# Kernel tuning notes

Measured on AMD Instinct MI355X. Metric: run time of the kernel, lower is better.

Reference implementation:

```python
import jax, jax.numpy as jnp
import numpy as np

N, E, F_IN, HID, OUT, H = 50000, 500000, 128, 64, 64, 2
P_DROP = 0.2


def setup_inputs() -> dict:
    key = jax.random.key(0)
    ks = jax.random.split(key, 24)
    g = lambda k, shp: jax.random.normal(k, shp, jnp.float32) * 0.05
    inp = {
        "feat": jax.random.normal(ks[0], (N, F_IN), jnp.float32),
        "edge_src": jax.random.randint(ks[1], (E,), 0, N, jnp.int32),
        "edge_dst": jax.random.randint(ks[2], (E,), 0, N, jnp.int32),
        # feature-mask linears
        "Wmt": g(ks[3], (F_IN, F_IN)), "bmt": g(ks[4], (F_IN,)),
        "Wms": g(ks[5], (F_IN, F_IN)), "bms": g(ks[6], (F_IN,)),
        # SAGEConv layers (mean aggregator): self + neigh linear + bias
        "W1_self": g(ks[7], (F_IN, HID)), "W1_neigh": g(ks[8], (F_IN, HID)), "b1": g(ks[9], (HID,)),
        "W2_self": g(ks[10], (HID, OUT)), "W2_neigh": g(ks[11], (HID, OUT)), "b2": g(ks[12], (OUT,)),
        # GATv2Conv layers: fc_src, fc_dst, attn vector per head, bias
        "g1_Wsrc": g(ks[13], (F_IN, H * HID)), "g1_Wdst": g(ks[14], (F_IN, H * HID)),
        "g1_attn": g(ks[15], (H, HID)), "g1_bias": g(ks[16], (H * HID,)),
        "g2_Wsrc": g(ks[17], (HID, H * OUT)), "g2_Wdst": g(ks[18], (HID, H * OUT)),
        "g2_attn": g(ks[19], (H, OUT)), "g2_bias": g(ks[20], (H * OUT,)),
        # final projection
        "W3": g(ks[21], (OUT + F_IN, OUT)), "b3": g(ks[22], (OUT,)),
    }
    # deterministic (inverted) dropout masks, training=True, p=0.2
    keep = 1.0 - P_DROP
    km1, km2 = jax.random.split(ks[23])
    inp["drop_t"] = jax.random.bernoulli(km1, keep, (N, HID)).astype(jnp.float32) / keep
    inp["drop_s"] = jax.random.bernoulli(km2, keep, (N, HID)).astype(jnp.float32) / keep
    return inp


def _sage_mean(h, src, dst, W_self, W_neigh, b):
    # mean over in-neighbors, then linear (mean and linear commute)
    agg = jax.ops.segment_sum(h[src], dst, num_segments=N)          # [N,D]
    deg = jax.ops.segment_sum(jnp.ones((E,), h.dtype), dst, num_segments=N)
    h_neigh = agg / jnp.maximum(deg, 1.0)[:, None]
    return h @ W_self + h_neigh @ W_neigh + b


def _gatv2(h, src, dst, Wsrc, Wdst, attn, bias, heads, dout):
    fs = (h @ Wsrc).reshape(N, heads, dout)
    fd = (h @ Wdst).reshape(N, heads, dout)
    e = jax.nn.leaky_relu(fs[src] + fd[dst], 0.2)                   # [E,H,D]
    logits = jnp.einsum('ehd,hd->eh', e, attn)                      # [E,H]
    m = jax.ops.segment_max(logits, dst, num_segments=N)            # edge softmax per dst
    ex = jnp.exp(logits - m[dst])
    denom = jax.ops.segment_sum(ex, dst, num_segments=N)
    alpha = ex / denom[dst]                                         # [E,H]
    out = jax.ops.segment_sum(alpha[:, :, None] * fs[src], dst, num_segments=N)
    return out + bias.reshape(heads, dout)                          # [N,H,D]


def _l2norm(x):
    return x / jnp.maximum(jnp.linalg.norm(x, axis=1, keepdims=True), 1e-12)


def reference(feat, edge_src, edge_dst, Wmt, bmt, Wms, bms,
              W1_self, W1_neigh, b1, W2_self, W2_neigh, b2,
              g1_Wsrc, g1_Wdst, g1_attn, g1_bias,
              g2_Wsrc, g2_Wdst, g2_attn, g2_bias,
              W3, b3, drop_t, drop_s):
    gelu = lambda x: jax.nn.gelu(x, approximate=False)  # torch F.gelu default = exact erf
    # topology branch (SAGE)
    h_t = feat * jax.nn.sigmoid(feat @ Wmt + bmt)
    h_t = gelu(_sage_mean(h_t, edge_src, edge_dst, W1_self, W1_neigh, b1)) * drop_t
    h_t = gelu(_sage_mean(h_t, edge_src, edge_dst, W2_self, W2_neigh, b2))
    h_t = jnp.concatenate([h_t, feat], axis=1) @ W3 + b3
    h_t = _l2norm(jax.nn.leaky_relu(h_t, 0.01))
    # semantic branch (GATv2)
    h_s = feat * jax.nn.sigmoid(feat @ Wms + bms)
    h_s = gelu(_gatv2(h_s, edge_src, edge_dst, g1_Wsrc, g1_Wdst, g1_attn, g1_bias, H, HID)).mean(axis=1) * drop_s
    h_s = gelu(_gatv2(h_s, edge_src, edge_dst, g2_Wsrc, g2_Wdst, g2_attn, g2_bias, H, OUT)).mean(axis=1)
    h_s = _l2norm(h_s)
    return (h_t, h_s)
```

## Files before the change

### kernel.cpp

```cpp
#include <hip/hip_runtime.h>
#include <math.h>

constexpr int N_  = 50000;
constexpr int E_  = 500000;
constexpr int NB_ = (N_ + 255) / 256;

typedef unsigned short u16;
typedef unsigned int u32;
typedef short short8 __attribute__((ext_vector_type(8)));
typedef __bf16 bf16x8 __attribute__((ext_vector_type(8)));
typedef float f32x4 __attribute__((ext_vector_type(4)));
typedef short short4v __attribute__((ext_vector_type(4)));

#define DINL __device__ __forceinline__

DINL float gelu_f(float x) { return 0.5f * x * (1.f + erff(x * 0.70710678118654752f)); }
DINL float sigmoid_f(float x) { return 1.f / (1.f + expf(-x)); }
DINL u16 f2b(float x) {
  unsigned u = __float_as_uint(x);
  return (u16)((u + 0x7FFFu + ((u >> 16) & 1u)) >> 16);
}
DINL float b2f(u16 b) { return __uint_as_float(((unsigned)b) << 16); }

template <int CTRL>
DINL float dpp_add(float c) {
  int p = __builtin_amdgcn_update_dpp(0, __builtin_bit_cast(int, c), CTRL, 0xf, 0xf, false);
  return c + __builtin_bit_cast(float, p);
}
DINL float reduce16(float c) {
  c = dpp_add<0xB1>(c);
  c = dpp_add<0x4E>(c);
  c = dpp_add<0x141>(c);
  c = dpp_add<0x140>(c);
  return c;
}

__global__ void deg_int_kernel(const int* __restrict__ dst, int* __restrict__ deg) {
  int t = blockIdx.x * 256 + threadIdx.x;
  if (t < E_) atomicAdd(&deg[dst[t]], 1);
}

__global__ __launch_bounds__(256) void scan_local(const int* __restrict__ deg,
    int* __restrict__ rowptr, int* __restrict__ bsum) {
  __shared__ int sums[4];
  const int tid = threadIdx.x, lane = tid & 63, wid = tid >> 6;
  const int i = blockIdx.x * 256 + tid;
  int v = (i < N_) ? deg[i] : 0;
  int x = v;
#pragma unroll
  for (int o = 1; o < 64; o <<= 1) { int y = __shfl_up(x, o); if (lane >= o) x += y; }
  if (lane == 63) sums[wid] = x;
  __syncthreads();
  int woff = 0;
#pragma unroll
  for (int w = 0; w < 3; ++w) if (w < wid) woff += sums[w];
  if (i < N_) rowptr[i] = x - v + woff;
  if (tid == 255) bsum[blockIdx.x] = woff + x;
}

__global__ __launch_bounds__(256) void scan_block(const int* __restrict__ bsum,
                                                  int* __restrict__ bpre) {
  __shared__ int sums[4];
  const int tid = threadIdx.x, lane = tid & 63, wid = tid >> 6;
  int v = (tid < NB_) ? bsum[tid] : 0;
  int x = v;
#pragma unroll
  for (int o = 1; o < 64; o <<= 1) { int y = __shfl_up(x, o); if (lane >= o) x += y; }
  if (lane == 63) sums[wid] = x;
  __syncthreads();
  int woff = 0;
#pragma unroll
  for (int w = 0; w < 3; ++w) if (w < wid) woff += sums[w];
  if (tid < NB_) bpre[tid] = x - v + woff;
  if (tid == 255) bpre[NB_] = woff + x;
}

__global__ __launch_bounds__(256) void scan_add(int* __restrict__ rowptr,
                                                const int* __restrict__ bpre) {
  int i = blockIdx.x * 256 + threadIdx.x;
  if (i < N_) rowptr[i] += bpre[i >> 8];
  else if (i == N_) rowptr[N_] = bpre[NB_];
}

__global__ void csr_fill(const int* __restrict__ src, const int* __restrict__ dst,
                         const int* __restrict__ rowptr, int* __restrict__ cursor,
                         int* __restrict__ colsrc) {
  int e = blockIdx.x * 256 + threadIdx.x;
  if (e >= E_) return;
  int d = dst[e];
  int pos = rowptr[d] + atomicAdd(&cursor[d], 1);
  colsrc[pos] = src[e];
}

__global__ __launch_bounds__(256) void pack_feat(const float* __restrict__ f,
                                                 u16* __restrict__ o) {
  int t = blockIdx.x * 256 + threadIdx.x;
  float4 v = ((const float4*)f)[t];
  short4v r;
  r[0] = (short)f2b(v.x); r[1] = (short)f2b(v.y);
  r[2] = (short)f2b(v.z); r[3] = (short)f2b(v.w);
  ((short4v*)o)[t] = r;
}

__global__ __launch_bounds__(256) void pack_w(
    const float* __restrict__ Wmt, const float* __restrict__ Wms,
    const float* __restrict__ W1s, const float* __restrict__ W1n,
    const float* __restrict__ W2s, const float* __restrict__ W2n,
    const float* __restrict__ g1Ws, const float* __restrict__ g1Wd,
    const float* __restrict__ g2Ws, const float* __restrict__ g2Wd,
    const float* __restrict__ W3, u16* __restrict__ dst) {
  int e = blockIdx.x * 256 + threadIdx.x;
  const float *Wa, *Wb = nullptr;
  int K1, K2 = 0, Ca, Cb = 0, st;
  if (e < 16384)       { Wa = Wmt;  K1 = 128; Ca = 128;           st = 0; }
  else if (e < 32768)  { Wa = Wms;  K1 = 128; Ca = 128;           st = 16384; }
  else if (e < 49152)  { Wa = W1s;  Wb = W1n; K1 = 128; Ca = 64; Cb = 64; st = 32768; }
  else if (e < 57344)  { Wa = W2s;  Wb = W2n; K1 = 64;  Ca = 64; Cb = 64; st = 49152; }
  else if (e < 90112)  { Wa = g1Ws; Wb = g1Wd; K1 = 128; Ca = 128; Cb = 128; st = 57344; }
  else if (e < 106496) { Wa = g2Ws; Wb = g2Wd; K1 = 64;  Ca = 128; Cb = 128; st = 90112; }
  else                 { Wa = W3;   K1 = 192; Ca = 64;            st = 106496; }
  int el = e - st;
  int Kt = K1 + K2;
  int ct = el / (Kt * 16);
  int rem = el - ct * Kt * 16;
  int ks = rem >> 9, rem2 = rem & 511, lane = rem2 >> 3, j = rem2 & 7;
  int k = ks * 32 + ((lane >> 4) << 3) + j;
  int c = ct * 16 + (lane & 15);
  float v;
  if (k < K1) v = (c < Ca) ? Wa[k * Ca + c] : Wb[k * Cb + (c - Ca)];
  else        v = Wb[(k - K1) * Ca + c];
  dst[e] = f2b(v);
}

template <int K1, int K2, int C, int EPI>
__global__ __launch_bounds__(512) void gemm_mfma(
    const u16* __restrict__ A1, const u16* __restrict__ A2,
    const u16* __restrict__ Wp, const float* __restrict__ bias,
    const float* __restrict__ bias2, const float* __restrict__ mulf,
    void* __restrict__ outv, void* __restrict__ outv2) {
  constexpr int K = K1 + K2, KS = K / 32, CT4 = C / 64;
  constexpr int NCH1 = K1 / 8, NCH2 = K2 / 8;
  __shared__ u16 alds[64 * K];
  const int tid = threadIdx.x;
  const int w = tid >> 6, l = tid & 63;
  const int cq = w >> 1, rh = w & 1;
  const int wr0 = blockIdx.x * 64;

  short8 wfrag[KS][CT4];
#pragma unroll
  for (int ks = 0; ks < KS; ++ks)
#pragma unroll
    for (int c4 = 0; c4 < CT4; ++c4)
      wfrag[ks][c4] = *(const short8*)(Wp +
          ((size_t)((cq * CT4 + c4) * KS + ks) * 64 + l) * 8);

  for (int i = tid; i < 64 * NCH1; i += 512) {
    int rr = i / NCH1, kc = i % NCH1;
    int gr = wr0 + rr; if (gr >= N_) gr = N_ - 1;
    short8 v = *(const short8*)(A1 + (long)gr * K1 + kc * 8);
    *(short8*)&alds[rr * K + ((kc ^ (rr & 7)) << 3)] = v;
  }
  if constexpr (K2 > 0) {
    for (int i = tid; i < 64 * NCH2; i += 512) {
      int rr = i / NCH2, kc = i % NCH2;
      int gr = wr0 + rr; if (gr >= N_) gr = N_ - 1;
      short8 v = *(const short8*)(A2 + (long)gr * K2 + kc * 8);
      *(short8*)&alds[rr * K + (((NCH1 + kc) ^ (rr & 7)) << 3)] = v;
    }
  }
  __syncthreads();

  f32x4 acc[2][CT4];
#pragma unroll
  for (int rr = 0; rr < 2; ++rr)
#pragma unroll
    for (int c4 = 0; c4 < CT4; ++c4) acc[rr][c4] = (f32x4){0.f, 0.f, 0.f, 0.f};

#pragma unroll
  for (int ks = 0; ks < KS; ++ks) {
#pragma unroll
    for (int rr = 0; rr < 2; ++rr) {
      const int nr = (rh * 2 + rr) * 16 + (l & 15);
      const int ch = (ks * 4 + (l >> 4)) ^ (nr & 7);
      short8 av = *(const short8*)&alds[nr * K + (ch << 3)];
      bf16x8 bf = __builtin_bit_cast(bf16x8, av);
#pragma unroll
      for (int c4 = 0; c4 < CT4; ++c4)
        acc[rr][c4] = __builtin_amdgcn_mfma_f32_16x16x32_bf16(
            __builtin_bit_cast(bf16x8, wfrag[ks][c4]), bf, acc[rr][c4], 0, 0, 0);
    }
  }

  const int colq = (l >> 4) << 2;
  if constexpr (EPI == 0) {
    u16* out = (u16*)outv;
#pragma unroll
    for (int rr = 0; rr < 2; ++rr) {
      int row = wr0 + (rh * 2 + rr) * 16 + (l & 15);
      if (row >= N_) continue;
#pragma unroll
      for (int c4 = 0; c4 < CT4; ++c4) {
        int colb = (cq * CT4 + c4) * 16 + colq;
        short4v s;
#pragma unroll
        for (int r = 0; r < 4; ++r) s[r] = (short)f2b(acc[rr][c4][r]);
        *(short4v*)(out + (long)row * C + colb) = s;
      }
    }
  } else if constexpr (EPI == 4) {
    __shared__ float ssb[64][4];
    float* out = (float*)outv;
    const int colb = cq * 16 + colq;
    float4 bv = *(const float4*)(bias + colb);
    float xv[2][4];
#pragma unroll
    for (int rr = 0; rr < 2; ++rr) {
      float ss = 0.f;
#pragma unroll
      for (int r = 0; r < 4; ++r) {
        float x = acc[rr][0][r] + ((const float*)&bv)[r];
        x = fmaxf(x, 0.01f * x);
        xv[rr][r] = x; ss += x * x;
      }
      ss += __shfl_xor(ss, 16);
      ss += __shfl_xor(ss, 32);
      if (l < 16) ssb[(rh * 2 + rr) * 16 + l][cq] = ss;
    }
    __syncthreads();
#pragma unroll
    for (int rr = 0; rr < 2; ++rr) {
      int nl = (rh * 2 + rr) * 16 + (l & 15);
      int row = wr0 + nl;
      if (row >= N_) continue;
      float ss = ssb[nl][0] + ssb[nl][1] + ssb[nl][2] + ssb[nl][3];
      float sc = 1.f / fmaxf(sqrtf(ss), 1e-12f);
      float4 o;
#pragma unroll
      for (int r = 0; r < 4; ++r) ((float*)&o)[r] = xv[rr][r] * sc;
      *(float4*)(out + (long)row * 64 + colb) = o;
    }
  } else {
#pragma unroll
    for (int c4 = 0; c4 < CT4; ++c4) {
      const int ct = cq * CT4 + c4;
      const bool lo = ct < 8;
      u16* op = lo ? (u16*)outv : (u16*)outv2;
      const int ccb = (ct & 7) * 16 + colq;
      float4 bv = *(const float4*)((lo ? bias : bias2) + ccb);
#pragma unroll
      for (int rr = 0; rr < 2; ++rr) {
        int nl = (rh * 2 + rr) * 16 + (l & 15);
        int row = wr0 + nl;
        if (row >= N_) continue;
        int ch = (ccb >> 3) ^ (nl & 7);
        short4v fq = *(const short4v*)&alds[nl * K + (ch << 3) + (ccb & 7)];
        short4v s;
#pragma unroll
        for (int r = 0; r < 4; ++r) {
          float x = acc[rr][c4][r] + ((const float*)&bv)[r];
          float fv = b2f((u16)fq[r]);
          s[r] = (short)f2b(fv * sigmoid_f(x));
        }
        *(short4v*)(op + (long)row * 128 + ccb) = s;
      }
    }
  }
}

template <bool DROP>
__global__ __launch_bounds__(256) void gather_sage(const u16* __restrict__ qp,
    const int* __restrict__ rowptr, const int* __restrict__ colsrc,
    const float* __restrict__ bias, const float* __restrict__ drop,
    u16* __restrict__ out) {
  int node = blockIdx.x * 4 + (threadIdx.x >> 6);
  int l = threadIdx.x & 63;
  int ql = l & 15, qg = l >> 4;
  int beg = rowptr[node], end = rowptr[node + 1];
  const int off = 4 * ql;
  float a0 = 0.f, a1 = 0.f, a2 = 0.f, a3 = 0.f;
  float b0 = 0.f, b1 = 0.f, b2 = 0.f, b3 = 0.f;
  int j = beg;
  for (; j + 8 <= end; j += 8) {
    int s0 = colsrc[j + qg], s1 = colsrc[j + 4 + qg];
    uint2 v0 = *(const uint2*)(qp + (size_t)s0 * 128 + 64 + off);
    uint2 v1 = *(const uint2*)(qp + (size_t)s1 * 128 + 64 + off);
    a0 += b2f((u16)(v0.x & 0xffffu));
    a1 += b2f((u16)(v0.x >> 16));
    a2 += b2f((u16)(v0.y & 0xffffu));
    a3 += b2f((u16)(v0.y >> 16));
    b0 += b2f((u16)(v1.x & 0xffffu));
    b1 += b2f((u16)(v1.x >> 16));
    b2 += b2f((u16)(v1.y & 0xffffu));
    b3 += b2f((u16)(v1.y >> 16));
  }
  for (; j < end; j += 4) {
    int idx = j + qg;
    bool valid = idx < end;
    int s = colsrc[valid ? idx : end - 1];
    uint2 v = *(const uint2*)(qp + (size_t)s * 128 + 64 + off);
    if (!valid) { v.x = 0; v.y = 0; }
    a0 += b2f((u16)(v.x & 0xffffu));
    a1 += b2f((u16)(v.x >> 16));
    a2 += b2f((u16)(v.y & 0xffffu));
    a3 += b2f((u16)(v.y >> 16));
  }
  a0 += b0; a1 += b1; a2 += b2; a3 += b3;
  a0 += __shfl_xor(a0, 32); a1 += __shfl_xor(a1, 32);
  a2 += __shfl_xor(a2, 32); a3 += __shfl_xor(a3, 32);
  a0 += __shfl_xor(a0, 16); a1 += __shfl_xor(a1, 16);
  a2 += __shfl_xor(a2, 16); a3 += __shfl_xor(a3, 16);
  if (l < 16) {
    float inv = 1.f / fmaxf((float)(end - beg), 1.f);
    uint2 qv = *(const uint2*)(qp + (size_t)node * 128 + off);
    float4 bv = *(const float4*)(bias + off);
    float g0 = gelu_f(b2f((u16)(qv.x & 0xffffu)) + a0 * inv + bv.x);
    float g1 = gelu_f(b2f((u16)(qv.x >> 16))     + a1 * inv + bv.y);
    float g2 = gelu_f(b2f((u16)(qv.y & 0xffffu)) + a2 * inv + bv.z);
    float g3 = gelu_f(b2f((u16)(qv.y >> 16))     + a3 * inv + bv.w);
    if constexpr (DROP) {
      float4 dv = *(const float4*)(drop + (long)node * 64 + off);
      g0 *= dv.x; g1 *= dv.y; g2 *= dv.z; g3 *= dv.w;
    }
    short4v s;
    s[0] = (short)f2b(g0); s[1] = (short)f2b(g1);
    s[2] = (short)f2b(g2); s[3] = (short)f2b(g3);
    *(short4v*)(out + (long)node * 64 + off) = s;
  }
}

template <bool LAYER1>
__global__ __launch_bounds__(256) void gat_fused(const u16* __restrict__ fsfd,
    const int* __restrict__ rowptr, const int* __restrict__ colsrc,
    const float* __restrict__ attn, const float* __restrict__ bias,
    const float* __restrict__ drop, void* __restrict__ outv) {
  int node = blockIdx.x * 4 + (threadIdx.x >> 6);
  int l = threadIdx.x & 63;
  int hl = l & 31, half = l >> 5;
  const int off = 4 * hl;
  float4 av = *(const float4*)(attn + off);
  uint2 fdv = *(const uint2*)(fsfd + (size_t)node * 256 + 128 + off);
  float fd0 = b2f((u16)(fdv.x & 0xffffu)), fd1 = b2f((u16)(fdv.x >> 16));
  float fd2 = b2f((u16)(fdv.y & 0xffffu)), fd3 = b2f((u16)(fdv.y >> 16));
  float d_own = 0.f, acc0 = 0.f, acc1 = 0.f, acc2 = 0.f, acc3 = 0.f;

  auto edge = [&](uint2 v, float m) {
    float f0 = b2f((u16)(v.x & 0xffffu)), f1 = b2f((u16)(v.x >> 16));
    float f2 = b2f((u16)(v.y & 0xffffu)), f3 = b2f((u16)(v.y >> 16));
    float t0 = f0 + fd0, t1 = f1 + fd1, t2 = f2 + fd2, t3 = f3 + fd3;
    t0 = fmaxf(t0, 0.2f * t0); t1 = fmaxf(t1, 0.2f * t1);
    t2 = fmaxf(t2, 0.2f * t2); t3 = fmaxf(t3, 0.2f * t3);
    float c = t0 * av.x + t1 * av.y + t2 * av.z + t3 * av.w;
    c = reduce16(c);
    float e = __expf(c) * m;
    d_own += e;
    acc0 += e * f0; acc1 += e * f1; acc2 += e * f2; acc3 += e * f3;
  };

  const int beg = rowptr[node], end = rowptr[node + 1];
  int j = beg;
  for (; j + 8 <= end; j += 8) {
    int sa = colsrc[j + half],     sb = colsrc[j + 2 + half];
    int sc = colsrc[j + 4 + half], sd = colsrc[j + 6 + half];
    uint2 va = *(const uint2*)(fsfd + (size_t)sa * 256 + off);
    uint2 vb = *(const uint2*)(fsfd + (size_t)sb * 256 + off);
    uint2 vc = *(const uint2*)(fsfd + (size_t)sc * 256 + off);
    uint2 vd = *(const uint2*)(fsfd + (size_t)sd * 256 + off);
    edge(va, 1.f); edge(vb, 1.f); edge(vc, 1.f); edge(vd, 1.f);
  }
  for (; j < end; j += 2) {
    int idx = j + half;
    bool valid = idx < end;
    int s = colsrc[valid ? idx : end - 1];
    uint2 v = *(const uint2*)(fsfd + (size_t)s * 256 + off);
    if (!valid) { v.x = 0; v.y = 0; }
    edge(v, valid ? 1.f : 0.f);
  }

  acc0 += __shfl_xor(acc0, 32); acc1 += __shfl_xor(acc1, 32);
  acc2 += __shfl_xor(acc2, 32); acc3 += __shfl_xor(acc3, 32);
  d_own += __shfl_xor(d_own, 32);

  float4 bv = *(const float4*)(bias + off);
  float inv = d_own > 0.f ? 1.f / d_own : 0.f;
  float g0 = gelu_f(bv.x + acc0 * inv);
  float g1 = gelu_f(bv.y + acc1 * inv);
  float g2 = gelu_f(bv.z + acc2 * inv);
  float g3 = gelu_f(bv.w + acc3 * inv);
  float v0 = 0.5f * (g0 + __shfl_xor(g0, 16));
  float v1 = 0.5f * (g1 + __shfl_xor(g1, 16));
  float v2 = 0.5f * (g2 + __shfl_xor(g2, 16));
  float v3 = 0.5f * (g3 + __shfl_xor(g3, 16));
  if constexpr (LAYER1) {
    if (l < 16) {
      float4 dv = *(const float4*)(drop + (long)node * 64 + 4 * l);
      short4v s;
      s[0] = (short)f2b(v0 * dv.x); s[1] = (short)f2b(v1 * dv.y);
      s[2] = (short)f2b(v2 * dv.z); s[3] = (short)f2b(v3 * dv.w);
      *(short4v*)((u16*)outv + (long)node * 64 + 4 * l) = s;
    }
  } else {
    float ss = v0 * v0 + v1 * v1 + v2 * v2 + v3 * v3;
    ss = reduce16(ss);
    float sc = 1.f / fmaxf(sqrtf(ss), 1e-12f);
    if (l < 16) {
      float4 o; o.x = v0 * sc; o.y = v1 * sc; o.z = v2 * sc; o.w = v3 * sc;
      *(float4*)((float*)outv + (long)node * 64 + 4 * l) = o;
    }
  }
}

extern "C" void kernel_launch(void* const* d_in, const int* in_sizes, int n_in,
                              void* d_out, int out_size, void* d_ws, size_t ws_size,
                              hipStream_t stream) {
  const float* feat = (const float*)d_in[0];
  const int*   esrc = (const int*)d_in[1];
  const int*   edst = (const int*)d_in[2];
  const float* Wmt = (const float*)d_in[3],  *bmt = (const float*)d_in[4];
  const float* Wms = (const float*)d_in[5],  *bms = (const float*)d_in[6];
  const float* W1s = (const float*)d_in[7],  *W1n = (const float*)d_in[8],  *b1 = (const float*)d_in[9];
  const float* W2s = (const float*)d_in[10], *W2n = (const float*)d_in[11], *b2 = (const float*)d_in[12];
  const float* g1Ws = (const float*)d_in[13], *g1Wd = (const float*)d_in[14];
  const float* g1a  = (const float*)d_in[15], *g1b  = (const float*)d_in[16];
  const float* g2Ws = (const float*)d_in[17], *g2Wd = (const float*)d_in[18];
  const float* g2a  = (const float*)d_in[19], *g2b  = (const float*)d_in[20];
  const float* W3  = (const float*)d_in[21], *b3 = (const float*)d_in[22];
  const float* dropt = (const float*)d_in[23], *drops = (const float*)d_in[24];

  float* out_t = (float*)d_out;
  float* out_s = out_t + (long)N_ * 64;

  u16* wsh = (u16*)d_ws;
  u16* featbf = wsh;
  u16* hbuf_t = wsh +  6400000;
  u16* hbuf_s = wsh + 12800000;
  u16* qp1    = wsh + 19200000;
  u16* h1     = wsh + 25600000;
  u16* qp2    = wsh + 28800000;
  u16* h2     = wsh + 35200000;
  u16* hs1    = wsh + 38400000;
  u16* fsfd   = wsh + 41600000;
  u16* Wpk    = wsh + 54400000;
  int* degi   = (int*)(wsh + 54518784);
  int* cursor = degi + N_;
  int* rowptr = cursor + N_;
  int* colsrc = rowptr + N_ + 1;
  int* bsum   = colsrc + E_;
  int* bpre   = bsum + NB_;

  const u16* WpMT = Wpk;
  const u16* WpS1 = Wpk + 32768;
  const u16* WpS2 = Wpk + 49152;
  const u16* WpG1 = Wpk + 57344;
  const u16* WpG2 = Wpk + 90112;
  const u16* WpW3 = Wpk + 106496;

  constexpr int GB = (N_ + 63) / 64;

  (void)hipMemsetAsync(degi, 0, (size_t)(2 * N_) * sizeof(int), stream);
  deg_int_kernel<<<(E_ + 255) / 256, 256, 0, stream>>>(edst, degi);
  scan_local<<<NB_, 256, 0, stream>>>(degi, rowptr, bsum);
  scan_block<<<1, 256, 0, stream>>>(bsum, bpre);
  scan_add<<<(N_ + 256) / 256, 256, 0, stream>>>(rowptr, bpre);
  csr_fill<<<(E_ + 255) / 256, 256, 0, stream>>>(esrc, edst, rowptr, cursor, colsrc);
  pack_feat<<<N_ * 128 / 4 / 256, 256, 0, stream>>>(feat, featbf);
  pack_w<<<464, 256, 0, stream>>>(Wmt, Wms, W1s, W1n, W2s, W2n,
                                  g1Ws, g1Wd, g2Ws, g2Wd, W3, Wpk);

  gemm_mfma<128, 0, 256, 5><<<GB, 512, 0, stream>>>(featbf, nullptr, WpMT, bmt, bms,
                                                    nullptr, hbuf_t, hbuf_s);

  gemm_mfma<128, 0, 128, 0><<<GB, 512, 0, stream>>>(hbuf_t, nullptr, WpS1, nullptr, nullptr,
                                                    nullptr, qp1, nullptr);
  gather_sage<true><<<N_ / 4, 256, 0, stream>>>(qp1, rowptr, colsrc, b1, dropt, h1);
  gemm_mfma<64, 0, 128, 0><<<GB, 512, 0, stream>>>(h1, nullptr, WpS2, nullptr, nullptr,
                                                   nullptr, qp2, nullptr);
  gather_sage<false><<<N_ / 4, 256, 0, stream>>>(qp2, rowptr, colsrc, b2, nullptr, h2);
  gemm_mfma<64, 128, 64, 4><<<GB, 512, 0, stream>>>(h2, featbf, WpW3, b3, nullptr,
                                                    nullptr, out_t, nullptr);

  gemm_mfma<128, 0, 256, 0><<<GB, 512, 0, stream>>>(hbuf_s, nullptr, WpG1, nullptr, nullptr,
                                                    nullptr, fsfd, nullptr);
  gat_fused<true><<<N_ / 4, 256, 0, stream>>>(fsfd, rowptr, colsrc, g1a, g1b, drops, hs1);
  gemm_mfma<64, 0, 256, 0><<<GB, 512, 0, stream>>>(hs1, nullptr, WpG2, nullptr, nullptr,
                                                   nullptr, fsfd, nullptr);
  gat_fused<false><<<N_ / 4, 256, 0, stream>>>(fsfd, rowptr, colsrc, g2a, g2b, nullptr, out_s);
}
```

Measured before the change: 272.3 us.

## Merge independent SAGE and GAT branch launches into combined multi-role kernels

Independent kernels are merged into single launches that pick a role from the block index. Degree counting, feature packing and weight packing share one prep kernel. The CSR fill runs alongside the mask GEMM, the SAGE and GAT GEMMs run in one launch per layer, and the SAGE and GAT gathers share one launch per layer. The goal is fewer launches and less idle tail time between small kernels, at the cost of mixed-role blocks whose register and shared-memory use is sized for the largest role, which may lower occupancy.

New measurement: 244.9 us. 10.1% less time.

```diff
diff --git a/kernel.cpp b/kernel.cpp
--- a/kernel.cpp
+++ b/kernel.cpp
@@ -4,6 +4,11 @@
 constexpr int N_  = 50000;
 constexpr int E_  = 500000;
 constexpr int NB_ = (N_ + 255) / 256;
+constexpr int GB_  = (N_ + 63) / 64;
+constexpr int NGB_ = N_ / 4;
+constexpr int DEGB_ = (E_ + 255) / 256;
+constexpr int PFB_  = N_ * 128 / 4 / 256;
+constexpr int CSRB_ = (E_ + 511) / 512;
 
 typedef unsigned short u16;
 typedef unsigned int u32;
@@ -33,11 +38,6 @@
   c = dpp_add<0x141>(c);
   c = dpp_add<0x140>(c);
   return c;
-}
-
-__global__ void deg_int_kernel(const int* __restrict__ dst, int* __restrict__ deg) {
-  int t = blockIdx.x * 256 + threadIdx.x;
-  if (t < E_) atomicAdd(&deg[dst[t]], 1);
 }
 
 __global__ __launch_bounds__(256) void scan_local(const int* __restrict__ deg,
@@ -82,69 +82,60 @@
   else if (i == N_) rowptr[N_] = bpre[NB_];
 }
 
-__global__ void csr_fill(const int* __restrict__ src, const int* __restrict__ dst,
-                         const int* __restrict__ rowptr, int* __restrict__ cursor,
-                         int* __restrict__ colsrc) {
-  int e = blockIdx.x * 256 + threadIdx.x;
-  if (e >= E_) return;
-  int d = dst[e];
-  int pos = rowptr[d] + atomicAdd(&cursor[d], 1);
-  colsrc[pos] = src[e];
-}
-
-__global__ __launch_bounds__(256) void pack_feat(const float* __restrict__ f,
-                                                 u16* __restrict__ o) {
-  int t = blockIdx.x * 256 + threadIdx.x;
-  float4 v = ((const float4*)f)[t];
-  short4v r;
-  r[0] = (short)f2b(v.x); r[1] = (short)f2b(v.y);
-  r[2] = (short)f2b(v.z); r[3] = (short)f2b(v.w);
-  ((short4v*)o)[t] = r;
-}
-
-__global__ __launch_bounds__(256) void pack_w(
+__global__ __launch_bounds__(256) void prep_kernel(
+    const int* __restrict__ edst, int* __restrict__ degi,
+    const float* __restrict__ feat, u16* __restrict__ featbf,
     const float* __restrict__ Wmt, const float* __restrict__ Wms,
     const float* __restrict__ W1s, const float* __restrict__ W1n,
     const float* __restrict__ W2s, const float* __restrict__ W2n,
     const float* __restrict__ g1Ws, const float* __restrict__ g1Wd,
     const float* __restrict__ g2Ws, const float* __restrict__ g2Wd,
-    const float* __restrict__ W3, u16* __restrict__ dst) {
-  int e = blockIdx.x * 256 + threadIdx.x;
-  const float *Wa, *Wb = nullptr;
-  int K1, K2 = 0, Ca, Cb = 0, st;
-  if (e < 16384)       { Wa = Wmt;  K1 = 128; Ca = 128;           st = 0; }
-  else if (e < 32768)  { Wa = Wms;  K1 = 128; Ca = 128;           st = 16384; }
-  else if (e < 49152)  { Wa = W1s;  Wb = W1n; K1 = 128; Ca = 64; Cb = 64; st = 32768; }
-  else if (e < 57344)  { Wa = W2s;  Wb = W2n; K1 = 64;  Ca = 64; Cb = 64; st = 49152; }
-  else if (e < 90112)  { Wa = g1Ws; Wb = g1Wd; K1 = 128; Ca = 128; Cb = 128; st = 57344; }
-  else if (e < 106496) { Wa = g2Ws; Wb = g2Wd; K1 = 64;  Ca = 128; Cb = 128; st = 90112; }
-  else                 { Wa = W3;   K1 = 192; Ca = 64;            st = 106496; }
-  int el = e - st;
-  int Kt = K1 + K2;
-  int ct = el / (Kt * 16);
-  int rem = el - ct * Kt * 16;
-  int ks = rem >> 9, rem2 = rem & 511, lane = rem2 >> 3, j = rem2 & 7;
-  int k = ks * 32 + ((lane >> 4) << 3) + j;
-  int c = ct * 16 + (lane & 15);
-  float v;
-  if (k < K1) v = (c < Ca) ? Wa[k * Ca + c] : Wb[k * Cb + (c - Ca)];
-  else        v = Wb[(k - K1) * Ca + c];
-  dst[e] = f2b(v);
+    const float* __restrict__ W3, u16* __restrict__ Wpk) {
+  int b = blockIdx.x, tid = threadIdx.x;
+  if (b < DEGB_) {
+    int t = b * 256 + tid;
+    if (t < E_) atomicAdd(&degi[edst[t]], 1);
+  } else if (b < DEGB_ + PFB_) {
+    int t = (b - DEGB_) * 256 + tid;
+    float4 v = ((const float4*)feat)[t];
+    short4v r;
+    r[0] = (short)f2b(v.x); r[1] = (short)f2b(v.y);
+    r[2] = (short)f2b(v.z); r[3] = (short)f2b(v.w);
+    ((short4v*)featbf)[t] = r;
+  } else {
+    int e = (b - DEGB_ - PFB_) * 256 + tid;
+    const float *Wa, *Wb = nullptr;
+    int K1, Ca, Cb = 0, st;
+    if (e < 16384)       { Wa = Wmt;  K1 = 128; Ca = 128;           st = 0; }
+    else if (e < 32768)  { Wa = Wms;  K1 = 128; Ca = 128;           st = 16384; }
+    else if (e < 49152)  { Wa = W1s;  Wb = W1n; K1 = 128; Ca = 64; Cb = 64; st = 32768; }
+    else if (e < 57344)  { Wa = W2s;  Wb = W2n; K1 = 64;  Ca = 64; Cb = 64; st = 49152; }
+    else if (e < 90112)  { Wa = g1Ws; Wb = g1Wd; K1 = 128; Ca = 128; Cb = 128; st = 57344; }
+    else if (e < 106496) { Wa = g2Ws; Wb = g2Wd; K1 = 64;  Ca = 128; Cb = 128; st = 90112; }
+    else                 { Wa = W3;   K1 = 192; Ca = 64;            st = 106496; }
+    int el = e - st;
+    int ct = el / (K1 * 16);
+    int rem = el - ct * K1 * 16;
+    int ks = rem >> 9, rem2 = rem & 511, lane = rem2 >> 3, j = rem2 & 7;
+    int k = ks * 32 + ((lane >> 4) << 3) + j;
+    int c = ct * 16 + (lane & 15);
+    float v = (c < Ca) ? Wa[k * Ca + c] : Wb[k * Cb + (c - Ca)];
+    Wpk[e] = f2b(v);
+  }
 }
 
 template <int K1, int K2, int C, int EPI>
-__global__ __launch_bounds__(512) void gemm_mfma(
+DINL void gemm_body(int bid, u16* alds,
     const u16* __restrict__ A1, const u16* __restrict__ A2,
     const u16* __restrict__ Wp, const float* __restrict__ bias,
-    const float* __restrict__ bias2, const float* __restrict__ mulf,
-    void* __restrict__ outv, void* __restrict__ outv2) {
+    const float* __restrict__ bias2, void* __restrict__ outv,
+    void* __restrict__ outv2) {
   constexpr int K = K1 + K2, KS = K / 32, CT4 = C / 64;
   constexpr int NCH1 = K1 / 8, NCH2 = K2 / 8;
-  __shared__ u16 alds[64 * K];
   const int tid = threadIdx.x;
   const int w = tid >> 6, l = tid & 63;
   const int cq = w >> 1, rh = w & 1;
-  const int wr0 = blockIdx.x * 64;
+  const int wr0 = bid * 64;
 
   short8 wfrag[KS][CT4];
 #pragma unroll
@@ -206,38 +197,6 @@
         for (int r = 0; r < 4; ++r) s[r] = (short)f2b(acc[rr][c4][r]);
         *(short4v*)(out + (long)row * C + colb) = s;
       }
-    }
-  } else if constexpr (EPI == 4) {
-    __shared__ float ssb[64][4];
-    float* out = (float*)outv;
-    const int colb = cq * 16 + colq;
-    float4 bv = *(const float4*)(bias + colb);
-    float xv[2][4];
-#pragma unroll
-    for (int rr = 0; rr < 2; ++rr) {
-      float ss = 0.f;
-#pragma unroll
-      for (int r = 0; r < 4; ++r) {
-        float x = acc[rr][0][r] + ((const float*)&bv)[r];
-        x = fmaxf(x, 0.01f * x);
-        xv[rr][r] = x; ss += x * x;
-      }
-      ss += __shfl_xor(ss, 16);
-      ss += __shfl_xor(ss, 32);
-      if (l < 16) ssb[(rh * 2 + rr) * 16 + l][cq] = ss;
-    }
-    __syncthreads();
-#pragma unroll
-    for (int rr = 0; rr < 2; ++rr) {
-      int nl = (rh * 2 + rr) * 16 + (l & 15);
-      int row = wr0 + nl;
-      if (row >= N_) continue;
-      float ss = ssb[nl][0] + ssb[nl][1] + ssb[nl][2] + ssb[nl][3];
-      float sc = 1.f / fmaxf(sqrtf(ss), 1e-12f);
-      float4 o;
-#pragma unroll
-      for (int r = 0; r < 4; ++r) ((float*)&o)[r] = xv[rr][r] * sc;
-      *(float4*)(out + (long)row * 64 + colb) = o;
     }
   } else {
 #pragma unroll
@@ -267,12 +226,122 @@
   }
 }
 
+__global__ __launch_bounds__(512) void stage0(
+    const u16* __restrict__ featbf, const u16* __restrict__ WpMT,
+    const float* __restrict__ bmt, const float* __restrict__ bms,
+    u16* __restrict__ hbuf_t, u16* __restrict__ hbuf_s,
+    const int* __restrict__ esrc, const int* __restrict__ edst,
+    const int* __restrict__ rowptr, int* __restrict__ cursor,
+    int* __restrict__ colsrc) {
+  __shared__ u16 alds[64 * 128];
+  int b = blockIdx.x;
+  if (b < GB_) {
+    gemm_body<128, 0, 256, 5>(b, alds, featbf, nullptr, WpMT, bmt, bms, hbuf_t, hbuf_s);
+  } else {
+    int e = (b - GB_) * 512 + threadIdx.x;
+    if (e < E_) {
+      int d = edst[e];
+      int pos = rowptr[d] + atomicAdd(&cursor[d], 1);
+      colsrc[pos] = esrc[e];
+    }
+  }
+}
+
+template <int KA, int KB>
+__global__ __launch_bounds__(512) void gemm_pair(
+    const u16* __restrict__ A_a, const u16* __restrict__ Wp_a, u16* __restrict__ out_a,
+    const u16* __restrict__ A_b, const u16* __restrict__ Wp_b, u16* __restrict__ out_b) {
+  __shared__ u16 alds[64 * 128];
+  int b = blockIdx.x;
+  if (b < GB_) gemm_body<KA, 0, 128, 0>(b, alds, A_a, nullptr, Wp_a, nullptr, nullptr, out_a, nullptr);
+  else         gemm_body<KB, 0, 256, 0>(b - GB_, alds, A_b, nullptr, Wp_b, nullptr, nullptr, out_b, nullptr);
+}
+
+__global__ __launch_bounds__(512) void final_t(
+    const u16* __restrict__ A1, const u16* __restrict__ A2,
+    const u16* __restrict__ Wp, const float* __restrict__ bias,
+    float* __restrict__ out) {
+  constexpr int K1 = 64, K2 = 128, K = 192, KS = 6;
+  constexpr int NCH1 = 8, NCH2 = 16;
+  __shared__ u16 alds[64 * K];
+  __shared__ float ssb[64][4];
+  const int tid = threadIdx.x;
+  const int w = tid >> 6, l = tid & 63;
+  const int cq = w >> 1, rh = w & 1;
+  const int wr0 = blockIdx.x * 64;
+
+  short8 wfrag[KS];
+#pragma unroll
+  for (int ks = 0; ks < KS; ++ks)
+    wfrag[ks] = *(const short8*)(Wp + ((size_t)(cq * KS + ks) * 64 + l) * 8);
+
+  for (int i = tid; i < 64 * NCH1; i += 512) {
+    int rr = i / NCH1, kc = i % NCH1;
+    int gr = wr0 + rr; if (gr >= N_) gr = N_ - 1;
+    short8 v = *(const short8*)(A1 + (long)gr * K1 + kc * 8);
+    *(short8*)&alds[rr * K + ((kc ^ (rr & 7)) << 3)] = v;
+  }
+  for (int i = tid; i < 64 * NCH2; i += 512) {
+    int rr = i / NCH2, kc = i % NCH2;
+    int gr = wr0 + rr; if (gr >= N_) gr = N_ - 1;
+    short8 v = *(const short8*)(A2 + (long)gr * K2 + kc * 8);
+    *(short8*)&alds[rr * K + (((NCH1 + kc) ^ (rr & 7)) << 3)] = v;
+  }
+  __syncthreads();
+
+  f32x4 acc[2];
+  acc[0] = (f32x4){0.f, 0.f, 0.f, 0.f};
+  acc[1] = (f32x4){0.f, 0.f, 0.f, 0.f};
+#pragma unroll
+  for (int ks = 0; ks < KS; ++ks) {
+#pragma unroll
+    for (int rr = 0; rr < 2; ++rr) {
+      const int nr = (rh * 2 + rr) * 16 + (l & 15);
+      const int ch = (ks * 4 + (l >> 4)) ^ (nr & 7);
+      short8 av = *(const short8*)&alds[nr * K + (ch << 3)];
+      acc[rr] = __builtin_amdgcn_mfma_f32_16x16x32_bf16(
+          __builtin_bit_cast(bf16x8, wfrag[ks]),
+          __builtin_bit_cast(bf16x8, av), acc[rr], 0, 0, 0);
+    }
+  }
+
+  const int colq = (l >> 4) << 2;
+  const int colb = cq * 16 + colq;
+  float4 bv = *(const float4*)(bias + colb);
+  float xv[2][4];
+#pragma unroll
+  for (int rr = 0; rr < 2; ++rr) {
+    float ss = 0.f;
+#pragma unroll
+    for (int r = 0; r < 4; ++r) {
+      float x = acc[rr][r] + ((const float*)&bv)[r];
+      x = fmaxf(x, 0.01f * x);
+      xv[rr][r] = x; ss += x * x;
+    }
+    ss += __shfl_xor(ss, 16);
+    ss += __shfl_xor(ss, 32);
+    if (l < 16) ssb[(rh * 2 + rr) * 16 + l][cq] = ss;
+  }
+  __syncthreads();
+#pragma unroll
+  for (int rr = 0; rr < 2; ++rr) {
+    int nl = (rh * 2 + rr) * 16 + (l & 15);
+    int row = wr0 + nl;
+    if (row >= N_) continue;
+    float ss = ssb[nl][0] + ssb[nl][1] + ssb[nl][2] + ssb[nl][3];
+    float sc = 1.f / fmaxf(sqrtf(ss), 1e-12f);
+    float4 o;
+#pragma unroll
+    for (int r = 0; r < 4; ++r) ((float*)&o)[r] = xv[rr][r] * sc;
+    *(float4*)(out + (long)row * 64 + colb) = o;
+  }
+}
+
 template <bool DROP>
-__global__ __launch_bounds__(256) void gather_sage(const u16* __restrict__ qp,
+DINL void sage_body(int node, const u16* __restrict__ qp,
     const int* __restrict__ rowptr, const int* __restrict__ colsrc,
     const float* __restrict__ bias, const float* __restrict__ drop,
     u16* __restrict__ out) {
-  int node = blockIdx.x * 4 + (threadIdx.x >> 6);
   int l = threadIdx.x & 63;
   int ql = l & 15, qg = l >> 4;
   int beg = rowptr[node], end = rowptr[node + 1];
@@ -329,11 +398,10 @@
 }
 
 template <bool LAYER1>
-__global__ __launch_bounds__(256) void gat_fused(const u16* __restrict__ fsfd,
+DINL void gat_body(int node, const u16* __restrict__ fsfd,
     const int* __restrict__ rowptr, const int* __restrict__ colsrc,
     const float* __restrict__ attn, const float* __restrict__ bias,
     const float* __restrict__ drop, void* __restrict__ outv) {
-  int node = blockIdx.x * 4 + (threadIdx.x >> 6);
   int l = threadIdx.x & 63;
   int hl = l & 31, half = l >> 5;
   const int off = 4 * hl;
@@ -409,6 +477,24 @@
   }
 }
 
+template <bool LAYER1, bool DROP>
+__global__ __launch_bounds__(256) void gather_stage(
+    const u16* __restrict__ fsfd, const u16* __restrict__ qp,
+    const int* __restrict__ rowptr, const int* __restrict__ colsrc,
+    const float* __restrict__ attn, const float* __restrict__ gbias,
+    const float* __restrict__ sbias, const float* __restrict__ gdrop,
+    const float* __restrict__ sdrop, void* __restrict__ gout,
+    u16* __restrict__ sout) {
+  int b = blockIdx.x;
+  if (b < NGB_) {
+    int node = b * 4 + (threadIdx.x >> 6);
+    gat_body<LAYER1>(node, fsfd, rowptr, colsrc, attn, gbias, gdrop, gout);
+  } else {
+    int node = (b - NGB_) * 4 + (threadIdx.x >> 6);
+    sage_body<DROP>(node, qp, rowptr, colsrc, sbias, sdrop, sout);
+  }
+}
+
 extern "C" void kernel_launch(void* const* d_in, const int* in_sizes, int n_in,
                               void* d_out, int out_size, void* d_ws, size_t ws_size,
                               hipStream_t stream) {
@@ -454,34 +540,23 @@
   const u16* WpG2 = Wpk + 90112;
   const u16* WpW3 = Wpk + 106496;
 
-  constexpr int GB = (N_ + 63) / 64;
-
   (void)hipMemsetAsync(degi, 0, (size_t)(2 * N_) * sizeof(int), stream);
-  deg_int_kernel<<<(E_ + 255) / 256, 256, 0, stream>>>(edst, degi);
+  prep_kernel<<<DEGB_ + PFB_ + 464, 256, 0, stream>>>(edst, degi, feat, featbf,
+      Wmt, Wms, W1s, W1n, W2s, W2n, g1Ws, g1Wd, g2Ws, g2Wd, W3, Wpk);
   scan_local<<<NB_, 256, 0, stream>>>(degi, rowptr, bsum);
   scan_block<<<1, 256, 0, stream>>>(bsum, bpre);
   scan_add<<<(N_ + 256) / 256, 256, 0, stream>>>(rowptr, bpre);
-  csr_fill<<<(E_ + 255) / 256, 256, 0, stream>>>(esrc, edst, rowptr, cursor, colsrc);
-  pack_feat<<<N_ * 128 / 4 / 256, 256, 0, stream>>>(feat, featbf);
-  pack_w<<<464, 256, 0, stream>>>(Wmt, Wms, W1s, W1n, W2s, W2n,
-                                  g1Ws, g1Wd, g2Ws, g2Wd, W3, Wpk);
-
-  gemm_mfma<128, 0, 256, 5><<<GB, 512, 0, stream>>>(featbf, nullptr, WpMT, bmt, bms,
-                                                    nullptr, hbuf_t, hbuf_s);
-
-  gemm_mfma<128, 0, 128, 0><<<GB, 512, 0, stream>>>(hbuf_t, nullptr, WpS1, nullptr, nullptr,
-                                                    nullptr, qp1, nullptr);
-  gather_sage<true><<<N_ / 4, 256, 0, stream>>>(qp1, rowptr, colsrc, b1, dropt, h1);
-  gemm_mfma<64, 0, 128, 0><<<GB, 512, 0, stream>>>(h1, nullptr, WpS2, nullptr, nullptr,
-                                                   nullptr, qp2, nullptr);
-  gather_sage<false><<<N_ / 4, 256, 0, stream>>>(qp2, rowptr, colsrc, b2, nullptr, h2);
-  gemm_mfma<64, 128, 64, 4><<<GB, 512, 0, stream>>>(h2, featbf, WpW3, b3, nullptr,
-                                                    nullptr, out_t, nullptr);
-
-  gemm_mfma<128, 0, 256, 0><<<GB, 512, 0, stream>>>(hbuf_s, nullptr, WpG1, nullptr, nullptr,
-                                                    nullptr, fsfd, nullptr);
-  gat_fused<true><<<N_ / 4, 256, 0, stream>>>(fsfd, rowptr, colsrc, g1a, g1b, drops, hs1);
-  gemm_mfma<64, 0, 256, 0><<<GB, 512, 0, stream>>>(hs1, nullptr, WpG2, nullptr, nullptr,
-                                                   nullptr, fsfd, nullptr);
-  gat_fused<false><<<N_ / 4, 256, 0, stream>>>(fsfd, rowptr, colsrc, g2a, g2b, nullptr, out_s);
-}
+
+  stage0<<<GB_ + CSRB_, 512, 0, stream>>>(featbf, WpMT, bmt, bms, hbuf_t, hbuf_s,
+                                          esrc, edst, rowptr, cursor, colsrc);
+
+  gemm_pair<128, 128><<<2 * GB_, 512, 0, stream>>>(hbuf_t, WpS1, qp1,
+                                                   hbuf_s, WpG1, fsfd);
+  gather_stage<true, true><<<2 * NGB_, 256, 0, stream>>>(fsfd, qp1, rowptr, colsrc,
+      g1a, g1b, b1, drops, dropt, hs1, h1);
+  gemm_pair<64, 64><<<2 * GB_, 512, 0, stream>>>(h1, WpS2, qp2,
+                                                 hs1, WpG2, fsfd);
+  gather_stage<false, false><<<2 * NGB_, 256, 0, stream>>>(fsfd, qp2, rowptr, colsrc,
+      g2a, g2b, b2, nullptr, nullptr, out_s, h2);
+  final_t<<<GB_, 512, 0, stream>>>(h2, featbf, WpW3, b3, out_t);
+}
```
